# Performance work log

Measured on AMD Instinct MI355X. Metric: run time of the kernel, lower is better.

The kernel has to match this reference:

```python
import jax, jax.numpy as jnp
import numpy as np

B, NPER, F, D, E, NUM_STEPS = 256, 512, 256, 32, 524288, 4
N = B * NPER
INIT_TAU, TAU_SCALE, STEP_ALPHA = 0.1, 0.5, 5.0


def setup_inputs() -> dict:
    key = jax.random.key(0)
    ks = jax.random.split(key, 10)
    x_start = jax.random.uniform(ks[0], (N,), jnp.float32, 0.1, 1.0)   # strictly positive iterate
    x_solution = jax.random.uniform(ks[1], (N,), jnp.float32, 0.0, 1.0)
    q = jax.random.normal(ks[2], (N,), jnp.float32)
    edge_src = jax.random.randint(ks[3], (E,), 0, N, jnp.int32)
    edge_dst = jax.random.randint(ks[4], (E,), 0, N, jnp.int32)
    vals_batch = jnp.repeat(jnp.arange(B, dtype=jnp.int32), NPER)      # equal-sized graphs
    proj_matrix = jax.random.normal(ks[5], (B, NPER, F), jnp.float32) / np.float32(np.sqrt(NPER))
    W_in = jax.random.normal(ks[6], (2, D), jnp.float32) / np.float32(np.sqrt(2.0))
    b_in = jnp.zeros((D,), jnp.float32)
    W_msg = jax.random.normal(ks[7], (D, D), jnp.float32) / np.float32(np.sqrt(D))
    b_msg = jnp.zeros((D,), jnp.float32)
    W_out = jax.random.normal(ks[8], (D, 1), jnp.float32) / np.float32(np.sqrt(D))
    b_out = jnp.zeros((1,), jnp.float32)
    return {"x_start": x_start, "x_solution": x_solution, "q": q,
            "proj_matrix": proj_matrix, "W_in": W_in, "b_in": b_in,
            "W_msg": W_msg, "b_msg": b_msg, "W_out": W_out, "b_out": b_out,
            "edge_src": edge_src, "edge_dst": edge_dst, "vals_batch": vals_batch}


def _l1_normalize(x, batch):
    # per-graph L1 normalization: x / sum_i |x_i| over the graph segment
    s = jax.ops.segment_sum(jnp.abs(x), batch, num_segments=B)
    return x / (s[batch] + 1e-12)


def _line_search(x, d, batch, max_alpha):
    # largest per-graph alpha s.t. x + alpha*d >= 0, capped at max_alpha
    ratio = jnp.where(d < 0, x / jnp.maximum(-d, 1e-12), max_alpha)
    a = jnp.clip(jax.ops.segment_min(ratio, batch, num_segments=B), 0.0, max_alpha)
    return a[batch]  # gathered back to per-node


def _gnn(xs, q, edge_src, edge_dst, W_in, b_in, W_msg, b_msg, W_out, b_out):
    h = jax.nn.relu(jnp.stack([xs, q], axis=-1) @ W_in + b_in)      # [N, D]
    m = h[edge_src] @ W_msg + b_msg                                  # [E, D]
    agg = jax.ops.segment_sum(m, edge_dst, num_segments=N)          # [N, D]
    h2 = jax.nn.relu(h + agg)
    return h2 @ W_out[:, 0] + b_out[0]                               # [N]


def reference(x_start, x_solution, q, proj_matrix, W_in, b_in, W_msg, b_msg,
              W_out, b_out, edge_src, edge_dst, vals_batch):
    tau = INIT_TAU
    xs = x_start
    preds, labels = [], []
    for _ in range(NUM_STEPS):
        pred = _gnn(xs, q, edge_src, edge_dst, W_in, b_in, W_msg, b_msg, W_out, b_out)
        preds.append(pred)
        labels.append(_l1_normalize(x_solution - xs, vals_batch))
        p = _l1_normalize(jax.lax.stop_gradient(pred), vals_batch)   # .detach() in torch
        direction = p + 3.0 * tau / (xs + tau)
        tau = max(tau * TAU_SCALE, 1e-5)
        # to_dense_batch with equal graph sizes == reshape; project onto nullspace basis
        dd = direction.reshape(B, NPER)
        df = jnp.einsum('bnf,bn->bf', proj_matrix, dd)               # [B, F]
        pproj = jnp.einsum('bnf,bf->bn', proj_matrix, df).reshape(-1)  # [N]
        alpha = _line_search(xs, pproj, vals_batch, STEP_ALPHA) * 0.995
        xs = xs + alpha * pproj
    return jnp.stack(preds, axis=1), jnp.stack(labels, axis=1)       # each [N, NUM_STEPS]
```

## Files before the change

### kernel.cpp

```cpp
#include <hip/hip_runtime.h>

#define BB 256
#define NPER 512
#define FF 256
#define DD 32
#define EE 524288
#define NN (BB*NPER)
#define NSTEPS 4

__device__ __forceinline__ float bflo(unsigned u) { return __uint_as_float(u << 16); }
__device__ __forceinline__ float bfhi(unsigned u) { return __uint_as_float(u & 0xFFFF0000u); }
__device__ __forceinline__ unsigned rtn_bf16(unsigned u) {
    return (u + 0x7FFFu + ((u >> 16) & 1u)) >> 16;
}


__global__ __launch_bounds__(256) void k_prep(const float* __restrict__ Pf,
                                              unsigned short* __restrict__ Pbf,
                                              const float* __restrict__ xs0,
                                              const float* __restrict__ q,
                                              float2* __restrict__ xq,
                                              const int* __restrict__ edst,
                                              unsigned* __restrict__ deg) {
    size_t g = (size_t)blockIdx.x * 256 + threadIdx.x;
    size_t idx = g * 8;
    float4 a = *(const float4*)(Pf + idx);
    float4 c = *(const float4*)(Pf + idx + 4);
    uint4 o;
    o.x = rtn_bf16(__float_as_uint(a.x)) | (rtn_bf16(__float_as_uint(a.y)) << 16);
    o.y = rtn_bf16(__float_as_uint(a.z)) | (rtn_bf16(__float_as_uint(a.w)) << 16);
    o.z = rtn_bf16(__float_as_uint(c.x)) | (rtn_bf16(__float_as_uint(c.y)) << 16);
    o.w = rtn_bf16(__float_as_uint(c.z)) | (rtn_bf16(__float_as_uint(c.w)) << 16);
    *(uint4*)(Pbf + idx) = o;
    if (g < NN) { float2 v; v.x = xs0[g]; v.y = q[g]; xq[g] = v; }
    if (g < EE) atomicAdd(&deg[edst[g]], 1u);
}

__global__ void k_bsum(const unsigned* __restrict__ deg, unsigned* __restrict__ bsum) {
    __shared__ unsigned r[256];
    int t = threadIdx.x;
    r[t] = deg[blockIdx.x * 256 + t];
    __syncthreads();
    for (int o = 128; o > 0; o >>= 1) { if (t < o) r[t] += r[t + o]; __syncthreads(); }
    if (t == 0) bsum[blockIdx.x] = r[0];
}

__global__ void k_scanb(const unsigned* __restrict__ bsum, unsigned* __restrict__ bbase) {
    __shared__ unsigned r[512];
    int t = threadIdx.x;
    unsigned own = bsum[t];
    r[t] = own;
    __syncthreads();
    for (int o = 1; o < 512; o <<= 1) {
        unsigned v = (t >= o) ? r[t - o] : 0u;
        __syncthreads();
        r[t] += v;
        __syncthreads();
    }
    bbase[t] = r[t] - own;
}

__global__ void k_offsets(const unsigned* __restrict__ deg, const unsigned* __restrict__ bbase,
                          unsigned* __restrict__ rowstart, unsigned* __restrict__ cursor) {
    __shared__ unsigned r[256];
    int t = threadIdx.x;
    int i = blockIdx.x * 256 + t;
    unsigned d = deg[i];
    r[t] = d;
    __syncthreads();
    for (int o = 1; o < 256; o <<= 1) {
        unsigned v = (t >= o) ? r[t - o] : 0u;
        __syncthreads();
        r[t] += v;
        __syncthreads();
    }
    unsigned excl = r[t] - d + bbase[blockIdx.x];
    rowstart[i] = excl;
    cursor[i] = excl;
}

__global__ void k_fill(const int* __restrict__ src, const int* __restrict__ dst,
                       unsigned* __restrict__ cursor, int* __restrict__ csr_src) {
    int e = blockIdx.x * blockDim.x + threadIdx.x;
    unsigned pos = atomicAdd(&cursor[dst[e]], 1u);
    csr_src[pos] = src[e];
}


__global__ void k_node_g(const float2* __restrict__ xq,
                         const float* __restrict__ Win, const float* __restrict__ bin,
                         const unsigned* __restrict__ rowstart, const unsigned* __restrict__ deg,
                         const int* __restrict__ csr_src,
                         const float* __restrict__ Wmsg, const float* __restrict__ bmsg,
                         const float* __restrict__ Wout, const float* __restrict__ bout,
                         float* __restrict__ pred, float* __restrict__ out_preds, int step) {
    int tid = threadIdx.x;
    int d = tid & 31;
    int i = blockIdx.x * 8 + (tid >> 5);
    float w0 = Win[d], w1 = Win[DD + d], b0 = bin[d];
    float wcol[DD];
    #pragma unroll
    for (int k = 0; k < DD; ++k) wcol[k] = Wmsg[k * DD + d];
    unsigned rs = rowstart[i];
    unsigned dg = deg[i];
    unsigned nfull = dg < 32u ? dg : 32u;
    float xv = 0.f, qv = 0.f;
    if ((unsigned)d < nfull) {
        int sv = csr_src[rs + d];
        float2 v = xq[sv];
        xv = v.x; qv = v.y;
    }
    float s = 0.f;
    for (unsigned j = 0; j < nfull; ++j) {
        float xj = __shfl(xv, (int)j, 32);
        float qj = __shfl(qv, (int)j, 32);
        s += fmaxf(xj * w0 + qj * w1 + b0, 0.f);
    }
    for (unsigned j = 32; j < dg; ++j) {
        int sv = csr_src[rs + j];
        float2 v = xq[sv];
        s += fmaxf(v.x * w0 + v.y * w1 + b0, 0.f);
    }
    float2 self = xq[i];
    float hval = fmaxf(self.x * w0 + self.y * w1 + b0, 0.f);
    float agg = (float)dg * bmsg[d];
    #pragma unroll
    for (int k = 0; k < DD; ++k) agg += __shfl(s, k, 32) * wcol[k];
    float h2 = fmaxf(hval + agg, 0.f);
    float v = h2 * Wout[d];
    for (int o = 16; o > 0; o >>= 1) v += __shfl_down(v, o, 32);
    if (d == 0) {
        float pr = v + bout[0];
        pred[i] = pr;
        out_preds[i * NSTEPS + step] = pr;
    }
}

__global__ __launch_bounds__(256) void k_dfc(const unsigned short* __restrict__ Pbf,
                                             const float2* __restrict__ xq,
                                             const float* __restrict__ xsol,
                                             const float* __restrict__ pred,
                                             float* __restrict__ out_labels,
                                             float* __restrict__ df,
                                             float tau, int step) {
    __shared__ float dd_l[64];
    __shared__ float sl[4 * FF];
    __shared__ float redA[4], redB[4];
    int blk = blockIdx.x;
    int b = blk >> 3, s = blk & 7;
    int t = threadIdx.x;
    int w = t >> 6, lane = t & 63;
    int gbase = b * NPER;

    float x0 = xq[gbase + t].x;
    float x1 = xq[gbase + 256 + t].x;
    float r0 = xsol[gbase + t] - x0;
    float r1 = xsol[gbase + 256 + t] - x1;
    float a1 = fabsf(r0) + fabsf(r1);
    float a2 = fabsf(pred[gbase + t]) + fabsf(pred[gbase + 256 + t]);
    #pragma unroll
    for (int o = 32; o > 0; o >>= 1) {
        a1 += __shfl_down(a1, o, 64);
        a2 += __shfl_down(a2, o, 64);
    }
    if (lane == 0) { redA[w] = a1; redB[w] = a2; }
    __syncthreads();
    float Sr = 1e-12f + redA[0] + redA[1] + redA[2] + redA[3];
    float Sp = 1e-12f + redB[0] + redB[1] + redB[2] + redB[3];
    if (s == 0) {
        out_labels[(size_t)(gbase + t) * NSTEPS + step] = r0 / Sr;
        out_labels[(size_t)(gbase + 256 + t) * NSTEPS + step] = r1 / Sr;
    }
    if (t < 64) {
        int row = s * 64 + t;
        float xx = xq[gbase + row].x;
        dd_l[t] = pred[gbase + row] / Sp + 3.0f * tau / (xx + tau);
    }
    __syncthreads();

    size_t pbase = ((size_t)(gbase + s * 64 + w * 16)) * FF + 4 * lane;
    const uint2* Pr = (const uint2*)(Pbf + pbase);
    float4 acc = {0.f, 0.f, 0.f, 0.f};
    #pragma unroll
    for (int n = 0; n < 16; ++n) {
        uint2 pv = Pr[(size_t)n * 64];
        float sc = dd_l[w * 16 + n];
        acc.x += bflo(pv.x) * sc; acc.y += bfhi(pv.x) * sc;
        acc.z += bflo(pv.y) * sc; acc.w += bfhi(pv.y) * sc;
    }
    ((float4*)sl)[w * 64 + lane] = acc;
    __syncthreads();
    if (t < FF) {
        float v = sl[t] + sl[FF + t] + sl[2 * FF + t] + sl[3 * FF + t];
        atomicAdd(&df[(size_t)(step * BB + b) * FF + t], v);
    }
}

__global__ __launch_bounds__(1024) void k_ppu(const unsigned short* __restrict__ Pbf,
                                              const float* __restrict__ df,
                                              float2* __restrict__ xq,
                                              const float* __restrict__ xsol,
                                              float* __restrict__ out_labels,
                                              int step, int last) {
    __shared__ float x_l[NPER], pp_l[NPER], dfl[FF];
    __shared__ float wmin[16], red[16];
    int b = blockIdx.x;
    int t = threadIdx.x;
    int w = t >> 6, lane = t & 63;
    int gbase = b * NPER;
    if (t < FF) dfl[t] = df[(size_t)(step * BB + b) * FF + t];
    if (t < NPER) x_l[t] = xq[gbase + t].x;
    __syncthreads();

    float4 dfv = ((const float4*)dfl)[lane];
    const uint2* Pr = (const uint2*)(Pbf + ((size_t)(gbase + w * 32)) * FF + 4 * lane);
    float mloc = 5.0f;
    #pragma unroll
    for (int n = 0; n < 32; ++n) {
        uint2 pv = Pr[(size_t)n * 64];
        float pr = bflo(pv.x) * dfv.x + bfhi(pv.x) * dfv.y
                 + bflo(pv.y) * dfv.z + bfhi(pv.y) * dfv.w;
        #pragma unroll
        for (int o = 1; o < 64; o <<= 1) pr += __shfl_xor(pr, o, 64);
        int row = w * 32 + n;
        if (lane == 0) pp_l[row] = pr;
        float ratio = (pr < 0.f) ? (x_l[row] / fmaxf(-pr, 1e-12f)) : 5.0f;
        mloc = fminf(mloc, ratio);
    }
    if (lane == 0) wmin[w] = mloc;
    __syncthreads();
    float mm = wmin[0];
    #pragma unroll
    for (int k = 1; k < 16; ++k) mm = fminf(mm, wmin[k]);
    float alpha = fminf(fmaxf(mm, 0.f), 5.0f) * 0.995f;
    float xnew = 0.f;
    if (t < NPER) {
        xnew = x_l[t] + alpha * pp_l[t];
        xq[gbase + t].x = xnew;
    }
    if (last) {
        float r = 0.f, a1 = 0.f;
        if (t < NPER) { r = xsol[gbase + t] - xnew; a1 = fabsf(r); }
        #pragma unroll
        for (int o = 32; o > 0; o >>= 1) a1 += __shfl_down(a1, o, 64);
        if (lane == 0) red[w] = a1;
        __syncthreads();
        float Sr = 1e-12f;
        #pragma unroll
        for (int k = 0; k < 16; ++k) Sr += red[k];
        if (t < NPER) out_labels[(size_t)(gbase + t) * NSTEPS + (NSTEPS - 1)] = r / Sr;
    }
}


extern "C" void kernel_launch(void* const* d_in, const int* in_sizes, int n_in,
                              void* d_out, int out_size, void* d_ws, size_t ws_size,
                              hipStream_t stream) {
    const float* x_start = (const float*)d_in[0];
    const float* x_sol   = (const float*)d_in[1];
    const float* q       = (const float*)d_in[2];
    const float* P       = (const float*)d_in[3];
    const float* Win     = (const float*)d_in[4];
    const float* bin     = (const float*)d_in[5];
    const float* Wmsg    = (const float*)d_in[6];
    const float* bmsg    = (const float*)d_in[7];
    const float* Wout    = (const float*)d_in[8];
    const float* bout    = (const float*)d_in[9];
    const int*   esrc    = (const int*)d_in[10];
    const int*   edst    = (const int*)d_in[11];

    float* out_preds  = (float*)d_out;
    float* out_labels = (float*)d_out + (size_t)NN * NSTEPS;

    float* w = (float*)d_ws;
    unsigned* deg = (unsigned*)w;      w += NN;
    float* df     = w;                 w += (size_t)3 * BB * FF;
    float2* xq  = (float2*)w; w += 2 * (size_t)NN;
    float* pred  = w; w += NN;
    unsigned* rowstart = (unsigned*)w; w += NN;
    unsigned* cursor   = (unsigned*)w; w += NN;
    unsigned* bsum     = (unsigned*)w; w += NN / 256;
    unsigned* bbase    = (unsigned*)w; w += NN / 256;
    int* csr_src       = (int*)w;      w += EE;
    unsigned short* Pbf = (unsigned short*)w;

    hipMemsetAsync(deg, 0, (NN + (size_t)3 * BB * FF) * sizeof(unsigned), stream);
    k_prep<<<(NN / 256) * (FF / 8), 256, 0, stream>>>(P, Pbf, x_start, q, xq, edst, deg);
    k_bsum<<<NN / 256, 256, 0, stream>>>(deg, bsum);
    k_scanb<<<1, NN / 256, 0, stream>>>(bsum, bbase);
    k_offsets<<<NN / 256, 256, 0, stream>>>(deg, bbase, rowstart, cursor);
    k_fill<<<EE / 256, 256, 0, stream>>>(esrc, edst, cursor, csr_src);

    float tau = 0.1f;
    for (int step = 0; step < NSTEPS; ++step) {
        k_node_g<<<NN / 8, 256, 0, stream>>>(xq, Win, bin, rowstart, deg, csr_src,
                                             Wmsg, bmsg, Wout, bout, pred, out_preds, step);
        if (step < NSTEPS - 1) {
            k_dfc<<<BB * 8, 256, 0, stream>>>(Pbf, xq, x_sol, pred, out_labels, df, tau, step);
            k_ppu<<<BB, 1024, 0, stream>>>(Pbf, df, xq, x_sol, out_labels,
                                           step, step == NSTEPS - 2 ? 1 : 0);
        }
        tau = fmaxf(tau * 0.5f, 1e-5f);
    }
}
```

Before: 525.4 us.

## Fuse bf16 conversion into first projection pass and simplify CSR build

The standalone prep pass that converted the 128MB fp32 projection matrix to bf16 is removed. The first k_dfc step now reads fp32 P directly, uses it, and writes the bf16 copy, which saves one full read of P. The three-kernel degree scan is replaced by a single kernel that gets per-block bases from a global atomic counter, so CSR rows are no longer globally ordered but stay contiguous. The df reduction switches from atomics to per-slice partial sums that k_ppu adds up, which also drops the memset of df, and k_node_g is templated on the step index.

```diff
diff --git a/kernel.cpp b/kernel.cpp
--- a/kernel.cpp
+++ b/kernel.cpp
@@ -15,54 +15,20 @@
 }
 
 
-__global__ __launch_bounds__(256) void k_prep(const float* __restrict__ Pf,
-                                              unsigned short* __restrict__ Pbf,
-                                              const float* __restrict__ xs0,
-                                              const float* __restrict__ q,
-                                              float2* __restrict__ xq,
-                                              const int* __restrict__ edst,
-                                              unsigned* __restrict__ deg) {
-    size_t g = (size_t)blockIdx.x * 256 + threadIdx.x;
-    size_t idx = g * 8;
-    float4 a = *(const float4*)(Pf + idx);
-    float4 c = *(const float4*)(Pf + idx + 4);
-    uint4 o;
-    o.x = rtn_bf16(__float_as_uint(a.x)) | (rtn_bf16(__float_as_uint(a.y)) << 16);
-    o.y = rtn_bf16(__float_as_uint(a.z)) | (rtn_bf16(__float_as_uint(a.w)) << 16);
-    o.z = rtn_bf16(__float_as_uint(c.x)) | (rtn_bf16(__float_as_uint(c.y)) << 16);
-    o.w = rtn_bf16(__float_as_uint(c.z)) | (rtn_bf16(__float_as_uint(c.w)) << 16);
-    *(uint4*)(Pbf + idx) = o;
-    if (g < NN) { float2 v; v.x = xs0[g]; v.y = q[g]; xq[g] = v; }
-    if (g < EE) atomicAdd(&deg[edst[g]], 1u);
-}
-
-__global__ void k_bsum(const unsigned* __restrict__ deg, unsigned* __restrict__ bsum) {
+__global__ void k_degpack(const int* __restrict__ dst, unsigned* __restrict__ deg,
+                          const float* __restrict__ xs0, const float* __restrict__ q,
+                          float2* __restrict__ xq) {
+    int t = blockIdx.x * blockDim.x + threadIdx.x;
+    if (t < NN) { float2 v; v.x = xs0[t]; v.y = q[t]; xq[t] = v; }
+    atomicAdd(&deg[dst[t]], 1u);
+}
+
+__global__ __launch_bounds__(256) void k_alloc(const unsigned* __restrict__ deg,
+                                               unsigned* __restrict__ gcur,
+                                               unsigned* __restrict__ rowstart,
+                                               unsigned* __restrict__ cursor) {
     __shared__ unsigned r[256];
-    int t = threadIdx.x;
-    r[t] = deg[blockIdx.x * 256 + t];
-    __syncthreads();
-    for (int o = 128; o > 0; o >>= 1) { if (t < o) r[t] += r[t + o]; __syncthreads(); }
-    if (t == 0) bsum[blockIdx.x] = r[0];
-}
-
-__global__ void k_scanb(const unsigned* __restrict__ bsum, unsigned* __restrict__ bbase) {
-    __shared__ unsigned r[512];
-    int t = threadIdx.x;
-    unsigned own = bsum[t];
-    r[t] = own;
-    __syncthreads();
-    for (int o = 1; o < 512; o <<= 1) {
-        unsigned v = (t >= o) ? r[t - o] : 0u;
-        __syncthreads();
-        r[t] += v;
-        __syncthreads();
-    }
-    bbase[t] = r[t] - own;
-}
-
-__global__ void k_offsets(const unsigned* __restrict__ deg, const unsigned* __restrict__ bbase,
-                          unsigned* __restrict__ rowstart, unsigned* __restrict__ cursor) {
-    __shared__ unsigned r[256];
+    __shared__ unsigned base;
     int t = threadIdx.x;
     int i = blockIdx.x * 256 + t;
     unsigned d = deg[i];
@@ -74,7 +40,9 @@
         r[t] += v;
         __syncthreads();
     }
-    unsigned excl = r[t] - d + bbase[blockIdx.x];
+    if (t == 255) base = atomicAdd(gcur, r[255]);
+    __syncthreads();
+    unsigned excl = r[t] - d + base;
     rowstart[i] = excl;
     cursor[i] = excl;
 }
@@ -87,13 +55,14 @@
 }
 
 
+template<int STEP>
 __global__ void k_node_g(const float2* __restrict__ xq,
                          const float* __restrict__ Win, const float* __restrict__ bin,
                          const unsigned* __restrict__ rowstart, const unsigned* __restrict__ deg,
                          const int* __restrict__ csr_src,
                          const float* __restrict__ Wmsg, const float* __restrict__ bmsg,
                          const float* __restrict__ Wout, const float* __restrict__ bout,
-                         float* __restrict__ pred, float* __restrict__ out_preds, int step) {
+                         float* __restrict__ pred, float* __restrict__ out_preds) {
     int tid = threadIdx.x;
     int d = tid & 31;
     int i = blockIdx.x * 8 + (tid >> 5);
@@ -132,16 +101,18 @@
     if (d == 0) {
         float pr = v + bout[0];
         pred[i] = pr;
-        out_preds[i * NSTEPS + step] = pr;
-    }
-}
-
-__global__ __launch_bounds__(256) void k_dfc(const unsigned short* __restrict__ Pbf,
+        out_preds[i * NSTEPS + STEP] = pr;
+    }
+}
+
+template<int STEP0>
+__global__ __launch_bounds__(256) void k_dfc(const float* __restrict__ Pf,
+                                             unsigned short* __restrict__ Pbf,
                                              const float2* __restrict__ xq,
                                              const float* __restrict__ xsol,
                                              const float* __restrict__ pred,
                                              float* __restrict__ out_labels,
-                                             float* __restrict__ df,
+                                             float* __restrict__ dfp,
                                              float tau, int step) {
     __shared__ float dd_l[64];
     __shared__ float sl[4 * FF];
@@ -179,25 +150,43 @@
     __syncthreads();
 
     size_t pbase = ((size_t)(gbase + s * 64 + w * 16)) * FF + 4 * lane;
-    const uint2* Pr = (const uint2*)(Pbf + pbase);
     float4 acc = {0.f, 0.f, 0.f, 0.f};
-    #pragma unroll
-    for (int n = 0; n < 16; ++n) {
-        uint2 pv = Pr[(size_t)n * 64];
-        float sc = dd_l[w * 16 + n];
-        acc.x += bflo(pv.x) * sc; acc.y += bfhi(pv.x) * sc;
-        acc.z += bflo(pv.y) * sc; acc.w += bfhi(pv.y) * sc;
+    if (STEP0) {
+        const float4* Pr = (const float4*)(Pf + pbase);
+        uint2* Pw = (uint2*)(Pbf + pbase);
+        #pragma unroll 4
+        for (int n = 0; n < 16; ++n) {
+            float4 pv = Pr[(size_t)n * 64];
+            float sc = dd_l[w * 16 + n];
+            acc.x += pv.x * sc; acc.y += pv.y * sc;
+            acc.z += pv.z * sc; acc.w += pv.w * sc;
+            unsigned u0 = rtn_bf16(__float_as_uint(pv.x));
+            unsigned u1 = rtn_bf16(__float_as_uint(pv.y));
+            unsigned u2 = rtn_bf16(__float_as_uint(pv.z));
+            unsigned u3 = rtn_bf16(__float_as_uint(pv.w));
+            uint2 o; o.x = u0 | (u1 << 16); o.y = u2 | (u3 << 16);
+            Pw[(size_t)n * 64] = o;
+        }
+    } else {
+        const uint2* Pr = (const uint2*)(Pbf + pbase);
+        #pragma unroll 8
+        for (int n = 0; n < 16; ++n) {
+            uint2 pv = Pr[(size_t)n * 64];
+            float sc = dd_l[w * 16 + n];
+            acc.x += bflo(pv.x) * sc; acc.y += bfhi(pv.x) * sc;
+            acc.z += bflo(pv.y) * sc; acc.w += bfhi(pv.y) * sc;
+        }
     }
     ((float4*)sl)[w * 64 + lane] = acc;
     __syncthreads();
     if (t < FF) {
         float v = sl[t] + sl[FF + t] + sl[2 * FF + t] + sl[3 * FF + t];
-        atomicAdd(&df[(size_t)(step * BB + b) * FF + t], v);
+        dfp[(size_t)((step * BB + b) * 8 + s) * FF + t] = v;
     }
 }
 
 __global__ __launch_bounds__(1024) void k_ppu(const unsigned short* __restrict__ Pbf,
-                                              const float* __restrict__ df,
+                                              const float* __restrict__ dfp,
                                               float2* __restrict__ xq,
                                               const float* __restrict__ xsol,
                                               float* __restrict__ out_labels,
@@ -208,7 +197,13 @@
     int t = threadIdx.x;
     int w = t >> 6, lane = t & 63;
     int gbase = b * NPER;
-    if (t < FF) dfl[t] = df[(size_t)(step * BB + b) * FF + t];
+    if (t < FF) {
+        const float* dp = dfp + (size_t)((step * BB + b) * 8) * FF + t;
+        float v = 0.f;
+        #pragma unroll
+        for (int s = 0; s < 8; ++s) v += dp[s * FF];
+        dfl[t] = v;
+    }
     if (t < NPER) x_l[t] = xq[gbase + t].x;
     __syncthreads();
 
@@ -273,31 +268,41 @@
     float* out_labels = (float*)d_out + (size_t)NN * NSTEPS;
 
     float* w = (float*)d_ws;
-    unsigned* deg = (unsigned*)w;      w += NN;
-    float* df     = w;                 w += (size_t)3 * BB * FF;
+    unsigned* deg  = (unsigned*)w; w += NN;
+    unsigned* gcur = (unsigned*)w; w += 2;
     float2* xq  = (float2*)w; w += 2 * (size_t)NN;
     float* pred  = w; w += NN;
+    float* dfp   = w; w += (size_t)3 * BB * 8 * FF;
     unsigned* rowstart = (unsigned*)w; w += NN;
     unsigned* cursor   = (unsigned*)w; w += NN;
-    unsigned* bsum     = (unsigned*)w; w += NN / 256;
-    unsigned* bbase    = (unsigned*)w; w += NN / 256;
     int* csr_src       = (int*)w;      w += EE;
     unsigned short* Pbf = (unsigned short*)w;
 
-    hipMemsetAsync(deg, 0, (NN + (size_t)3 * BB * FF) * sizeof(unsigned), stream);
-    k_prep<<<(NN / 256) * (FF / 8), 256, 0, stream>>>(P, Pbf, x_start, q, xq, edst, deg);
-    k_bsum<<<NN / 256, 256, 0, stream>>>(deg, bsum);
-    k_scanb<<<1, NN / 256, 0, stream>>>(bsum, bbase);
-    k_offsets<<<NN / 256, 256, 0, stream>>>(deg, bbase, rowstart, cursor);
+    hipMemsetAsync(deg, 0, (NN + 2) * sizeof(unsigned), stream);
+    k_degpack<<<EE / 256, 256, 0, stream>>>(edst, deg, x_start, q, xq);
+    k_alloc<<<NN / 256, 256, 0, stream>>>(deg, gcur, rowstart, cursor);
     k_fill<<<EE / 256, 256, 0, stream>>>(esrc, edst, cursor, csr_src);
 
     float tau = 0.1f;
     for (int step = 0; step < NSTEPS; ++step) {
-        k_node_g<<<NN / 8, 256, 0, stream>>>(xq, Win, bin, rowstart, deg, csr_src,
-                                             Wmsg, bmsg, Wout, bout, pred, out_preds, step);
+        switch (step) {
+        case 0: k_node_g<0><<<NN / 8, 256, 0, stream>>>(xq, Win, bin, rowstart, deg, csr_src,
+                                                        Wmsg, bmsg, Wout, bout, pred, out_preds); break;
+        case 1: k_node_g<1><<<NN / 8, 256, 0, stream>>>(xq, Win, bin, rowstart, deg, csr_src,
+                                                        Wmsg, bmsg, Wout, bout, pred, out_preds); break;
+        case 2: k_node_g<2><<<NN / 8, 256, 0, stream>>>(xq, Win, bin, rowstart, deg, csr_src,
+                                                        Wmsg, bmsg, Wout, bout, pred, out_preds); break;
+        default: k_node_g<3><<<NN / 8, 256, 0, stream>>>(xq, Win, bin, rowstart, deg, csr_src,
+                                                         Wmsg, bmsg, Wout, bout, pred, out_preds); break;
+        }
         if (step < NSTEPS - 1) {
-            k_dfc<<<BB * 8, 256, 0, stream>>>(Pbf, xq, x_sol, pred, out_labels, df, tau, step);
-            k_ppu<<<BB, 1024, 0, stream>>>(Pbf, df, xq, x_sol, out_labels,
+            if (step == 0)
+                k_dfc<1><<<BB * 8, 256, 0, stream>>>(P, Pbf, xq, x_sol, pred,
+                                                     out_labels, dfp, tau, step);
+            else
+                k_dfc<0><<<BB * 8, 256, 0, stream>>>(P, Pbf, xq, x_sol, pred,
+                                                     out_labels, dfp, tau, step);
+            k_ppu<<<BB, 1024, 0, stream>>>(Pbf, dfp, xq, x_sol, out_labels,
                                            step, step == NSTEPS - 2 ? 1 : 0);
         }
         tau = fmaxf(tau * 0.5f, 1e-5f);
```

After: 527.3 us. No clear change (+0.4%).
